# Optimization experiments

Measured on AMD Instinct MI355X. Metric: run time of the kernel, lower is better.

Reference implementation:

```python
import jax, jax.numpy as jnp
import numpy as np

N_NODES = 50000
N_EDGES = 500000
MUL0, MUL1 = 16, 8          # multiplicities of 0e and 1o irreps (in == out)
DIM = MUL0 + 3 * MUL1       # 40
N_BASIS, MID = 10, 32
WNUM = MUL0*MUL0 + MUL1*MUL0 + MUL0*MUL1 + MUL1*MUL1  # 576
INV_SQRT3 = 1.0 / np.sqrt(3.0)  # wigner-3j normalization for l=1 paths
FAN_IN = MUL0 + MUL1        # paths into each output irrep: 16 + 8 = 24
A0 = np.sqrt(1.0 / FAN_IN)  # sqrt((2*0+1)/fan_in)
A1 = np.sqrt(3.0 / FAN_IN)  # sqrt((2*1+1)/fan_in)
LN_EPS = 1e-5


def setup_inputs() -> dict:
    key = jax.random.key(0)
    ks = jax.random.split(key, 8)
    return {
        "x": jax.random.normal(ks[0], (N_NODES, DIM), jnp.float32),
        "edge_sh": jax.random.normal(ks[1], (N_EDGES, 4), jnp.float32),
        "edge_length_embedded": jax.random.uniform(ks[2], (N_EDGES, N_BASIS), jnp.float32),
        "W1": jax.random.normal(ks[3], (N_BASIS, MID), jnp.float32),
        "W2": jax.random.normal(ks[4], (MID, WNUM), jnp.float32),
        "gamma": jnp.ones((DIM,), jnp.float32),
        "beta": jnp.zeros((DIM,), jnp.float32),
        "edge_src": jax.random.randint(ks[5], (N_EDGES,), 0, N_NODES),
        "edge_dst": jax.random.randint(ks[6], (N_EDGES,), 0, N_NODES),
        "avg_num_neighbors": 10,
    }


def reference(x, edge_sh, edge_length_embedded, W1, W2, gamma, beta,
              edge_src, edge_dst, avg_num_neighbors):
    # radial MLP -> per-edge tensor-product weights (e3nn FullyConnectedNet style)
    h = jax.nn.silu(edge_length_embedded @ W1 / jnp.sqrt(jnp.float32(N_BASIS)))
    w = h @ W2 / jnp.sqrt(jnp.float32(MID))              # [E, 576]

    # gather node features onto edges and split into irrep blocks
    xg = x[edge_src]                                     # [E, 40]
    s = xg[:, :MUL0]                                     # [E, 16]  scalars 0e
    v = xg[:, MUL0:].reshape(-1, MUL1, 3)                # [E, 8, 3] vectors 1o
    sh0 = edge_sh[:, 0]                                  # [E]
    sh1 = edge_sh[:, 1:4]                                # [E, 3]

    # split per-edge weights by tensor-product path
    o0, o1, o2 = MUL0*MUL0, MUL0*MUL0 + MUL1*MUL0, MUL0*MUL0 + MUL1*MUL0 + MUL0*MUL1
    W_ss0 = w[:, :o0].reshape(-1, MUL0, MUL0)            # 0e x 0e -> 0e
    W_vv0 = w[:, o0:o1].reshape(-1, MUL1, MUL0)          # 1o x 1o -> 0e
    W_sv1 = w[:, o1:o2].reshape(-1, MUL0, MUL1)          # 0e x 1o -> 1o
    W_vs1 = w[:, o2:].reshape(-1, MUL1, MUL1)            # 1o x 0e -> 1o

    # weighted Clebsch-Gordan tensor product (per edge)
    vdot = jnp.einsum('eui,ei->eu', v, sh1) * INV_SQRT3  # CG 1x1->0
    out0 = A0 * (jnp.einsum('euk,eu->ek', W_ss0, s * sh0[:, None])
                 + jnp.einsum('euk,eu->ek', W_vv0, vdot))            # [E, 16]
    out1 = A1 * INV_SQRT3 * (
        jnp.einsum('euk,eu->ek', W_sv1, s)[:, :, None] * sh1[:, None, :]
        + jnp.einsum('euk,eui->eki', W_vs1, v) * sh0[:, None, None])  # [E, 8, 3]
    edge_values = jnp.concatenate([out0, out1.reshape(-1, 3 * MUL1)], axis=1)

    # scatter-sum into destination nodes, degree normalization, layernorm
    node = jax.ops.segment_sum(edge_values, edge_dst, num_segments=N_NODES)
    node = node / jnp.sqrt(jnp.float32(avg_num_neighbors))
    mu = node.mean(axis=-1, keepdims=True)
    var = node.var(axis=-1, keepdims=True)
    return (node - mu) * jax.lax.rsqrt(var + LN_EPS) * gamma + beta
```

## Files before the change

### kernel.cpp

```cpp
#include <hip/hip_runtime.h>
#include <hip/hip_bf16.h>

#define N_NODES 50000
#define N_EDGES 500000
#define MUL0 16
#define MUL1 8
#define DIM 40
#define N_BASIS 10
#define MID 32
#define WNUM 576
#define SCAN_BLOCKS 196
#define N_GROUPS (N_EDGES / 16)

typedef __attribute__((ext_vector_type(8))) short bf16x8_t;
typedef __attribute__((ext_vector_type(4))) float f32x4_t;

__device__ __forceinline__ float bf2f(unsigned short u) {
  return __uint_as_float(((unsigned int)u) << 16);
}
__device__ __forceinline__ unsigned short f2bf(float f) {
  unsigned int x = __float_as_uint(f);
  unsigned int r = x + 0x7fffu + ((x >> 16) & 1u);
  return (unsigned short)(r >> 16);
}
__device__ __forceinline__ bool detect_bf16(const void* gamma) {
  return ((const unsigned int*)gamma)[0] == 0x3F803F80u;
}
template <bool BF16>
__device__ __forceinline__ float ld(const void* p, size_t i) {
  if (BF16) return bf2f(((const unsigned short*)p)[i]);
  return ((const float*)p)[i];
}

#define C_INV_SQRT10 0.31622776601683794f
#define C_INV_SQRT32 0.17677669529663687f
#define C_INV_SQRT3  0.5773502691896258f
#define C_A0C        0.20412414523193154f

__device__ __forceinline__ f32x4_t mfma16x16x32(bf16x8_t a, bf16x8_t b, f32x4_t c) {
  return __builtin_amdgcn_mfma_f32_16x16x32_bf16(a, b, c, 0, 0, 0);
}


__global__ __launch_bounds__(256) void hist_kernel(
    const int* __restrict__ edge_dst, int* __restrict__ cnt) {
  int e = blockIdx.x * 256 + threadIdx.x;
  if (e < N_EDGES) atomicAdd(&cnt[edge_dst[e]], 1);
}

__global__ __launch_bounds__(256) void scanA_kernel(
    const int* __restrict__ cnt, int* __restrict__ off, int* __restrict__ btot) {
  __shared__ int s[256];
  const int tid = threadIdx.x;
  const int i = blockIdx.x * 256 + tid;
  int v = (i < N_NODES) ? cnt[i] : 0;
  s[tid] = v;
  __syncthreads();
  for (int d = 1; d < 256; d <<= 1) {
    int t = (tid >= d) ? s[tid - d] : 0;
    __syncthreads();
    s[tid] += t;
    __syncthreads();
  }
  if (i < N_NODES) off[i] = s[tid] - v;
  if (tid == 255) btot[blockIdx.x] = s[255];
}

__global__ __launch_bounds__(256) void scanB_kernel(
    const int* __restrict__ btot, int* __restrict__ bbase) {
  __shared__ int s[256];
  const int tid = threadIdx.x;
  int v = (tid < SCAN_BLOCKS) ? btot[tid] : 0;
  s[tid] = v;
  __syncthreads();
  for (int d = 1; d < 256; d <<= 1) {
    int t = (tid >= d) ? s[tid - d] : 0;
    __syncthreads();
    s[tid] += t;
    __syncthreads();
  }
  if (tid < SCAN_BLOCKS) bbase[tid] = s[tid] - v;
}

__global__ __launch_bounds__(256) void scanC_kernel(
    int* __restrict__ off, const int* __restrict__ bbase) {
  const int i = blockIdx.x * 256 + threadIdx.x;
  if (i < N_NODES) off[i] += bbase[blockIdx.x];
}

__global__ __launch_bounds__(256) void scatter_kernel(
    const int* __restrict__ edge_dst, const int* __restrict__ off,
    int* __restrict__ fill, int* __restrict__ eids) {
  int e = blockIdx.x * 256 + threadIdx.x;
  if (e >= N_EDGES) return;
  int d = edge_dst[e];
  int pos = off[d] + atomicAdd(&fill[d], 1);
  eids[pos] = e;
}


template <bool BF16>
__device__ void edge_mfma_body(
    const void* __restrict__ x,
    const void* __restrict__ edge_sh,
    const void* __restrict__ elemb,
    const void* __restrict__ W1,
    const void* __restrict__ W2,
    const int* __restrict__ edge_src,
    unsigned short* __restrict__ ev,
    short* __restrict__ w2b, float* __restrict__ w1s, float* __restrict__ stg)
{
  const int tid = threadIdx.x;

  for (int i = tid; i < 36 * 512; i += 256) {
    int m = i / WNUM;
    int col = i - m * WNUM;
    int q = m >> 3, j = m & 7;
    int t = col >> 4, n = col & 15;
    short val;
    if (BF16) val = (short)((const unsigned short*)W2)[i];
    else      val = (short)f2bf(((const float*)W2)[i]);
    w2b[t * 512 + q * 128 + n * 8 + j] = val;
  }
  for (int i = tid; i < N_BASIS * MID; i += 256) w1s[i] = ld<BF16>(W1, i);
  __syncthreads();

  const int lane = tid & 63;
  const int wid  = tid >> 6;
  const int quad = lane >> 4;
  const int l16  = lane & 15;
  float* S = stg + wid * 1504;

  for (int gi = blockIdx.x * 4 + wid; gi < N_GROUPS; gi += gridDim.x * 4) {
    const int e0 = gi * 16;

    if (lane < 16) {
      if (BF16) {
        uint2 sw = *reinterpret_cast<const uint2*>(
            (const unsigned short*)edge_sh + (size_t)(e0 + lane) * 4);
        S[0 * 16 + lane] = __uint_as_float(sw.x << 16);
        S[1 * 16 + lane] = __uint_as_float(sw.x & 0xffff0000u);
        S[2 * 16 + lane] = __uint_as_float(sw.y << 16);
        S[3 * 16 + lane] = __uint_as_float(sw.y & 0xffff0000u);
      } else {
        float4 s4 = *reinterpret_cast<const float4*>(
            (const float*)edge_sh + (size_t)(e0 + lane) * 4);
        S[0 * 16 + lane] = s4.x; S[1 * 16 + lane] = s4.y;
        S[2 * 16 + lane] = s4.z; S[3 * 16 + lane] = s4.w;
      }
    }

    {
      const int src = edge_src[e0 + l16];
      if (BF16) {
        const uint4* xr = reinterpret_cast<const uint4*>(
            (const unsigned short*)x + (size_t)src * DIM);
        uint4 c = xr[quad];
        unsigned wv[4] = {c.x, c.y, c.z, c.w};
        #pragma unroll
        for (int p = 0; p < 4; ++p) {
          int col = quad * 8 + 2 * p;
          float lo = __uint_as_float(wv[p] << 16);
          float hi = __uint_as_float(wv[p] & 0xffff0000u);
          int off0 = (col < 16) ? (64 + col * 16) : (448 + (col - 16) * 16);
          int off1 = (col + 1 < 16) ? (64 + (col + 1) * 16) : (448 + (col - 15) * 16);
          S[off0 + l16] = lo;
          S[off1 + l16] = hi;
        }
        if (lane < 16) {
          uint4 c4 = xr[4];
          unsigned wv4[4] = {c4.x, c4.y, c4.z, c4.w};
          #pragma unroll
          for (int p = 0; p < 4; ++p) {
            int col = 32 + 2 * p;
            S[448 + (col - 16) * 16 + lane] = __uint_as_float(wv4[p] << 16);
            S[448 + (col - 15) * 16 + lane] = __uint_as_float(wv4[p] & 0xffff0000u);
          }
        }
      } else {
        const float4* xr = reinterpret_cast<const float4*>(
            (const float*)x + (size_t)src * DIM);
        #pragma unroll
        for (int cc = 0; cc < 2; ++cc) {
          int c = quad + cc * 4;
          float4 t = xr[c];
          float vv[4] = {t.x, t.y, t.z, t.w};
          #pragma unroll
          for (int p = 0; p < 4; ++p) {
            int col = 4 * c + p;
            int offp = (col < 16) ? (64 + col * 16) : (448 + (col - 16) * 16);
            S[offp + l16] = vv[p];
          }
        }
        if (quad < 2) {
          int c = 8 + quad;
          float4 t = xr[c];
          float vv[4] = {t.x, t.y, t.z, t.w};
          #pragma unroll
          for (int p = 0; p < 4; ++p) {
            int col = 4 * c + p;
            S[448 + (col - 16) * 16 + l16] = vv[p];
          }
        }
      }
    }
    __builtin_amdgcn_wave_barrier();

    #pragma unroll
    for (int p = 0; p < 2; ++p) {
      int idx = lane + p * 64;
      int u = idx >> 4, e = idx & 15;
      float vdv = (S[448 + (u * 3 + 0) * 16 + e] * S[16 + e] +
                   S[448 + (u * 3 + 1) * 16 + e] * S[32 + e] +
                   S[448 + (u * 3 + 2) * 16 + e] * S[48 + e]) * C_INV_SQRT3;
      S[320 + u * 16 + e] = vdv;
    }
    __builtin_amdgcn_wave_barrier();

    bf16x8_t af;
    {
      float eb[N_BASIS];
      if (BF16) {
        const unsigned short* er = (const unsigned short*)elemb + (size_t)(e0 + l16) * N_BASIS;
        #pragma unroll
        for (int p = 0; p < 5; ++p) {
          unsigned uv = *reinterpret_cast<const unsigned*>(er + p * 2);
          eb[2 * p]     = __uint_as_float(uv << 16);
          eb[2 * p + 1] = __uint_as_float(uv & 0xffff0000u);
        }
      } else {
        const float* er = (const float*)elemb + (size_t)(e0 + l16) * N_BASIS;
        #pragma unroll
        for (int p = 0; p < 5; ++p) {
          float2 fv = *reinterpret_cast<const float2*>(er + p * 2);
          eb[2 * p] = fv.x; eb[2 * p + 1] = fv.y;
        }
      }
      #pragma unroll
      for (int j = 0; j < 8; ++j) {
        int k = quad * 8 + j;
        float p = 0.f;
        #pragma unroll
        for (int b = 0; b < N_BASIS; ++b) p += eb[b] * w1s[b * MID + k];
        float z = p * C_INV_SQRT10;
        float hh = z / (1.f + __expf(-z)) * C_INV_SQRT32;
        af[j] = (short)f2bf(hh);
      }
    }

    f32x4_t s0 = *reinterpret_cast<const f32x4_t*>(&S[quad * 4]);

    f32x4_t out0 = {0.f, 0.f, 0.f, 0.f};
    f32x4_t tsv  = {0.f, 0.f, 0.f, 0.f};
    f32x4_t tv0  = {0.f, 0.f, 0.f, 0.f};
    f32x4_t tv1  = {0.f, 0.f, 0.f, 0.f};
    f32x4_t tv2  = {0.f, 0.f, 0.f, 0.f};
    const f32x4_t zero = {0.f, 0.f, 0.f, 0.f};
    const int usel = (l16 >> 3);

    #pragma unroll
    for (int t = 0; t < 16; ++t) {
      bf16x8_t bf = *reinterpret_cast<const bf16x8_t*>(&w2b[t * 512 + lane * 8]);
      f32x4_t D = mfma16x16x32(af, bf, zero);
      f32x4_t sv = *reinterpret_cast<const f32x4_t*>(&S[64 + t * 16 + quad * 4]);
      out0 += D * (sv * s0);
    }
    #pragma unroll
    for (int t = 0; t < 8; ++t) {
      bf16x8_t bf = *reinterpret_cast<const bf16x8_t*>(&w2b[(16 + t) * 512 + lane * 8]);
      f32x4_t D = mfma16x16x32(af, bf, zero);
      f32x4_t vdv = *reinterpret_cast<const f32x4_t*>(&S[320 + t * 16 + quad * 4]);
      out0 += D * vdv;
    }
    #pragma unroll
    for (int t = 0; t < 8; ++t) {
      bf16x8_t bf = *reinterpret_cast<const bf16x8_t*>(&w2b[(24 + t) * 512 + lane * 8]);
      f32x4_t D = mfma16x16x32(af, bf, zero);
      int u = 2 * t + usel;
      f32x4_t sv = *reinterpret_cast<const f32x4_t*>(&S[64 + u * 16 + quad * 4]);
      tsv += D * sv;
    }
    #pragma unroll
    for (int t = 0; t < 4; ++t) {
      bf16x8_t bf = *reinterpret_cast<const bf16x8_t*>(&w2b[(32 + t) * 512 + lane * 8]);
      f32x4_t D = mfma16x16x32(af, bf, zero);
      int u = 2 * t + usel;
      f32x4_t v0 = *reinterpret_cast<const f32x4_t*>(&S[448 + (u * 3 + 0) * 16 + quad * 4]);
      f32x4_t v1 = *reinterpret_cast<const f32x4_t*>(&S[448 + (u * 3 + 1) * 16 + quad * 4]);
      f32x4_t v2 = *reinterpret_cast<const f32x4_t*>(&S[448 + (u * 3 + 2) * 16 + quad * 4]);
      tv0 += D * v0; tv1 += D * v1; tv2 += D * v2;
    }

    #pragma unroll
    for (int r = 0; r < 4; ++r) {
      tsv[r] += __shfl_xor(tsv[r], 8, 64);
      tv0[r] += __shfl_xor(tv0[r], 8, 64);
      tv1[r] += __shfl_xor(tv1[r], 8, 64);
      tv2[r] += __shfl_xor(tv2[r], 8, 64);
    }

    #pragma unroll
    for (int r = 0; r < 4; ++r)
      S[832 + (quad * 4 + r) * 42 + l16] = C_A0C * out0[r];
    if (l16 < 8) {
      f32x4_t h1x = *reinterpret_cast<const f32x4_t*>(&S[16 + quad * 4]);
      f32x4_t h1y = *reinterpret_cast<const f32x4_t*>(&S[32 + quad * 4]);
      f32x4_t h1z = *reinterpret_cast<const f32x4_t*>(&S[48 + quad * 4]);
      #pragma unroll
      for (int r = 0; r < 4; ++r) {
        int rowb = 832 + (quad * 4 + r) * 42 + 16 + 3 * l16;
        S[rowb + 0] = C_A0C * (tsv[r] * h1x[r] + tv0[r] * s0[r]);
        S[rowb + 1] = C_A0C * (tsv[r] * h1y[r] + tv1[r] * s0[r]);
        S[rowb + 2] = C_A0C * (tsv[r] * h1z[r] + tv2[r] * s0[r]);
      }
    }
    __builtin_amdgcn_wave_barrier();

    unsigned* evout = reinterpret_cast<unsigned*>(ev + (size_t)e0 * DIM);
    #pragma unroll
    for (int sI = 0; sI < 5; ++sI) {
      int vidx = 2 * (lane + 64 * sI);
      int edge = vidx / 40, col = vidx - edge * 40;
      float2 pr = *reinterpret_cast<const float2*>(&S[832 + edge * 42 + col]);
      evout[lane + 64 * sI] = (unsigned)f2bf(pr.x) | ((unsigned)f2bf(pr.y) << 16);
    }
  }
}

__global__ __launch_bounds__(256, 2) void edge_mfma_kernel(
    const void* __restrict__ x,
    const void* __restrict__ edge_sh,
    const void* __restrict__ elemb,
    const void* __restrict__ W1,
    const void* __restrict__ W2,
    const void* __restrict__ gamma,
    const int* __restrict__ edge_src,
    unsigned short* __restrict__ ev)
{
  __shared__ __align__(16) short w2b[36 * 512];
  __shared__ __align__(16) float w1s[N_BASIS * MID];
  __shared__ __align__(16) float stg[4 * 1504];

  if (detect_bf16(gamma))
    edge_mfma_body<true >(x, edge_sh, elemb, W1, W2, edge_src, ev, w2b, w1s, stg);
  else
    edge_mfma_body<false>(x, edge_sh, elemb, W1, W2, edge_src, ev, w2b, w1s, stg);
}


template <bool BF16>
__device__ __forceinline__ void node_body(
    const unsigned short* __restrict__ ev,
    const int* __restrict__ eids,
    const int* __restrict__ cnt,
    const int* __restrict__ off,
    const void* __restrict__ gamma,
    const void* __restrict__ beta,
    const int* __restrict__ avg,
    void* __restrict__ out, int n)
{
  const int c = cnt[n];
  const int o = off[n];
  float s[DIM];
  #pragma unroll
  for (int d = 0; d < DIM; ++d) s[d] = 0.f;

  for (int j = 0; j < c; ++j) {
    int e = eids[o + j];
    const uint4* p = reinterpret_cast<const uint4*>(ev + (size_t)e * DIM);
    #pragma unroll
    for (int q = 0; q < 5; ++q) {
      uint4 t = p[q];
      unsigned int wl[4] = {t.x, t.y, t.z, t.w};
      #pragma unroll
      for (int r = 0; r < 4; ++r) {
        s[q * 8 + 2 * r]     += __uint_as_float(wl[r] << 16);
        s[q * 8 + 2 * r + 1] += __uint_as_float(wl[r] & 0xffff0000u);
      }
    }
  }

  const float inv = rsqrtf((float)avg[0]);
  float mean = 0.f;
  #pragma unroll
  for (int d = 0; d < DIM; ++d) { s[d] *= inv; mean += s[d]; }
  mean *= (1.f / DIM);
  float var = 0.f;
  #pragma unroll
  for (int d = 0; d < DIM; ++d) { float dd = s[d] - mean; var += dd * dd; }
  var *= (1.f / DIM);
  const float r = rsqrtf(var + 1e-5f);

  if (BF16) {
    #pragma unroll
    for (int d = 0; d < DIM; ++d) {
      float y = (s[d] - mean) * r * ld<true>(gamma, d) + ld<true>(beta, d);
      ((unsigned short*)out)[(size_t)n * DIM + d] = f2bf(y);
    }
  } else {
    float4* op = reinterpret_cast<float4*>((float*)out + (size_t)n * DIM);
    #pragma unroll
    for (int q = 0; q < 10; ++q) {
      float4 t;
      t.x = (s[q*4+0] - mean) * r * ld<false>(gamma, q*4+0) + ld<false>(beta, q*4+0);
      t.y = (s[q*4+1] - mean) * r * ld<false>(gamma, q*4+1) + ld<false>(beta, q*4+1);
      t.z = (s[q*4+2] - mean) * r * ld<false>(gamma, q*4+2) + ld<false>(beta, q*4+2);
      t.w = (s[q*4+3] - mean) * r * ld<false>(gamma, q*4+3) + ld<false>(beta, q*4+3);
      op[q] = t;
    }
  }
}

__global__ __launch_bounds__(256) void node_kernel(
    const unsigned short* __restrict__ ev,
    const int* __restrict__ eids,
    const int* __restrict__ cnt,
    const int* __restrict__ off,
    const void* __restrict__ gamma,
    const void* __restrict__ beta,
    const int* __restrict__ avg,
    void* __restrict__ out)
{
  const int n = blockIdx.x * blockDim.x + threadIdx.x;
  if (n >= N_NODES) return;
  if (detect_bf16(gamma)) node_body<true >(ev, eids, cnt, off, gamma, beta, avg, out, n);
  else                    node_body<false>(ev, eids, cnt, off, gamma, beta, avg, out, n);
}

extern "C" void kernel_launch(void* const* d_in, const int* in_sizes, int n_in,
                              void* d_out, int out_size, void* d_ws, size_t ws_size,
                              hipStream_t stream) {
  const void* x       = d_in[0];
  const void* edge_sh = d_in[1];
  const void* elemb   = d_in[2];
  const void* W1      = d_in[3];
  const void* W2      = d_in[4];
  const void* gamma   = d_in[5];
  const void* beta    = d_in[6];
  const int* edge_src = (const int*)d_in[7];
  const int* edge_dst = (const int*)d_in[8];
  const int* avg      = (const int*)d_in[9];

  char* wsb = (char*)d_ws;
  unsigned short* ev = (unsigned short*)(wsb);
  int* eids  = (int*)(wsb + 40000000);
  int* cnt   = (int*)(wsb + 42000000);
  int* off   = (int*)(wsb + 42200000);
  int* fill  = (int*)(wsb + 42400000);
  int* btot  = (int*)(wsb + 42600000);
  int* bbase = (int*)(wsb + 42600800);

  hipMemsetAsync(cnt, 0, 600000, stream);

  const int EB = (N_EDGES + 255) / 256;
  hist_kernel   <<<EB, 256, 0, stream>>>(edge_dst, cnt);
  scanA_kernel  <<<SCAN_BLOCKS, 256, 0, stream>>>(cnt, off, btot);
  scanB_kernel  <<<1, 256, 0, stream>>>(btot, bbase);
  scanC_kernel  <<<SCAN_BLOCKS, 256, 0, stream>>>(off, bbase);
  scatter_kernel<<<EB, 256, 0, stream>>>(edge_dst, off, fill, eids);

  edge_mfma_kernel<<<512, 256, 0, stream>>>(x, edge_sh, elemb, W1, W2, gamma,
                                            edge_src, ev);

  node_kernel<<<SCAN_BLOCKS, 256, 0, stream>>>(ev, eids, cnt, off,
                                               gamma, beta, avg, d_out);
}
```

Measured before the change: 239.1 us.

## Write edge values in destination-sorted order so node reduction reads contiguously

The position kernel now records each edge's slot in the CSR order rather than an edge-id list. The edge kernel scatters its bf16 output rows straight to those slots, so the node kernel reads each node's edges as one contiguous block without the eids indirection. The LDS staging buffer is shrunk by reusing the front of the per-wave area, which allows occupancy 3 and a 768-block grid. The cost is scattered 16-byte writes from the edge kernel in place of coalesced stores, plus extra wave barriers to guard the reused LDS.

```diff
diff --git a/kernel.cpp b/kernel.cpp
--- a/kernel.cpp
+++ b/kernel.cpp
@@ -88,14 +88,13 @@
   if (i < N_NODES) off[i] += bbase[blockIdx.x];
 }
 
-__global__ __launch_bounds__(256) void scatter_kernel(
+__global__ __launch_bounds__(256) void pos_kernel(
     const int* __restrict__ edge_dst, const int* __restrict__ off,
-    int* __restrict__ fill, int* __restrict__ eids) {
+    int* __restrict__ fill, int* __restrict__ epos) {
   int e = blockIdx.x * 256 + threadIdx.x;
   if (e >= N_EDGES) return;
   int d = edge_dst[e];
-  int pos = off[d] + atomicAdd(&fill[d], 1);
-  eids[pos] = e;
+  epos[e] = off[d] + atomicAdd(&fill[d], 1);
 }
 
 
@@ -107,6 +106,7 @@
     const void* __restrict__ W1,
     const void* __restrict__ W2,
     const int* __restrict__ edge_src,
+    const int* __restrict__ epos,
     unsigned short* __restrict__ ev,
     short* __restrict__ w2b, float* __restrict__ w1s, float* __restrict__ stg)
 {
@@ -129,10 +129,14 @@
   const int wid  = tid >> 6;
   const int quad = lane >> 4;
   const int l16  = lane & 15;
-  float* S = stg + wid * 1504;
+  float* S = stg + wid * 832;
 
   for (int gi = blockIdx.x * 4 + wid; gi < N_GROUPS; gi += gridDim.x * 4) {
     const int e0 = gi * 16;
+    __builtin_amdgcn_wave_barrier();
+
+    const int posA = epos[e0 + (lane >> 2)];
+    const int posB = (lane < 16) ? epos[e0 + lane] : 0;
 
     if (lane < 16) {
       if (BF16) {
@@ -298,17 +302,18 @@
       tv1[r] += __shfl_xor(tv1[r], 8, 64);
       tv2[r] += __shfl_xor(tv2[r], 8, 64);
     }
+    __builtin_amdgcn_wave_barrier();
 
     #pragma unroll
     for (int r = 0; r < 4; ++r)
-      S[832 + (quad * 4 + r) * 42 + l16] = C_A0C * out0[r];
+      S[64 + (quad * 4 + r) * 42 + l16] = C_A0C * out0[r];
     if (l16 < 8) {
       f32x4_t h1x = *reinterpret_cast<const f32x4_t*>(&S[16 + quad * 4]);
       f32x4_t h1y = *reinterpret_cast<const f32x4_t*>(&S[32 + quad * 4]);
       f32x4_t h1z = *reinterpret_cast<const f32x4_t*>(&S[48 + quad * 4]);
       #pragma unroll
       for (int r = 0; r < 4; ++r) {
-        int rowb = 832 + (quad * 4 + r) * 42 + 16 + 3 * l16;
+        int rowb = 64 + (quad * 4 + r) * 42 + 16 + 3 * l16;
         S[rowb + 0] = C_A0C * (tsv[r] * h1x[r] + tv0[r] * s0[r]);
         S[rowb + 1] = C_A0C * (tsv[r] * h1y[r] + tv1[r] * s0[r]);
         S[rowb + 2] = C_A0C * (tsv[r] * h1z[r] + tv2[r] * s0[r]);
@@ -316,18 +321,29 @@
     }
     __builtin_amdgcn_wave_barrier();
 
-    unsigned* evout = reinterpret_cast<unsigned*>(ev + (size_t)e0 * DIM);
-    #pragma unroll
-    for (int sI = 0; sI < 5; ++sI) {
-      int vidx = 2 * (lane + 64 * sI);
-      int edge = vidx / 40, col = vidx - edge * 40;
-      float2 pr = *reinterpret_cast<const float2*>(&S[832 + edge * 42 + col]);
-      evout[lane + 64 * sI] = (unsigned)f2bf(pr.x) | ((unsigned)f2bf(pr.y) << 16);
-    }
-  }
-}
-
-__global__ __launch_bounds__(256, 2) void edge_mfma_kernel(
+    {
+      const int edge = lane >> 2, chunk = lane & 3;
+      const float* rp = &S[64 + edge * 42 + chunk * 8];
+      unsigned p0 = (unsigned)f2bf(rp[0]) | ((unsigned)f2bf(rp[1]) << 16);
+      unsigned p1 = (unsigned)f2bf(rp[2]) | ((unsigned)f2bf(rp[3]) << 16);
+      unsigned p2 = (unsigned)f2bf(rp[4]) | ((unsigned)f2bf(rp[5]) << 16);
+      unsigned p3 = (unsigned)f2bf(rp[6]) | ((unsigned)f2bf(rp[7]) << 16);
+      uint4 t; t.x = p0; t.y = p1; t.z = p2; t.w = p3;
+      *reinterpret_cast<uint4*>(ev + (size_t)posA * DIM + chunk * 8) = t;
+      if (lane < 16) {
+        const float* rq = &S[64 + lane * 42 + 32];
+        unsigned q0 = (unsigned)f2bf(rq[0]) | ((unsigned)f2bf(rq[1]) << 16);
+        unsigned q1 = (unsigned)f2bf(rq[2]) | ((unsigned)f2bf(rq[3]) << 16);
+        unsigned q2 = (unsigned)f2bf(rq[4]) | ((unsigned)f2bf(rq[5]) << 16);
+        unsigned q3 = (unsigned)f2bf(rq[6]) | ((unsigned)f2bf(rq[7]) << 16);
+        uint4 t2; t2.x = q0; t2.y = q1; t2.z = q2; t2.w = q3;
+        *reinterpret_cast<uint4*>(ev + (size_t)posB * DIM + 32) = t2;
+      }
+    }
+  }
+}
+
+__global__ __launch_bounds__(256, 3) void edge_mfma_kernel(
     const void* __restrict__ x,
     const void* __restrict__ edge_sh,
     const void* __restrict__ elemb,
@@ -335,23 +351,23 @@
     const void* __restrict__ W2,
     const void* __restrict__ gamma,
     const int* __restrict__ edge_src,
+    const int* __restrict__ epos,
     unsigned short* __restrict__ ev)
 {
   __shared__ __align__(16) short w2b[36 * 512];
   __shared__ __align__(16) float w1s[N_BASIS * MID];
-  __shared__ __align__(16) float stg[4 * 1504];
+  __shared__ __align__(16) float stg[4 * 832];
 
   if (detect_bf16(gamma))
-    edge_mfma_body<true >(x, edge_sh, elemb, W1, W2, edge_src, ev, w2b, w1s, stg);
+    edge_mfma_body<true >(x, edge_sh, elemb, W1, W2, edge_src, epos, ev, w2b, w1s, stg);
   else
-    edge_mfma_body<false>(x, edge_sh, elemb, W1, W2, edge_src, ev, w2b, w1s, stg);
+    edge_mfma_body<false>(x, edge_sh, elemb, W1, W2, edge_src, epos, ev, w2b, w1s, stg);
 }
 
 
 template <bool BF16>
 __device__ __forceinline__ void node_body(
     const unsigned short* __restrict__ ev,
-    const int* __restrict__ eids,
     const int* __restrict__ cnt,
     const int* __restrict__ off,
     const void* __restrict__ gamma,
@@ -365,12 +381,11 @@
   #pragma unroll
   for (int d = 0; d < DIM; ++d) s[d] = 0.f;
 
+  const uint4* p = reinterpret_cast<const uint4*>(ev + (size_t)o * DIM);
   for (int j = 0; j < c; ++j) {
-    int e = eids[o + j];
-    const uint4* p = reinterpret_cast<const uint4*>(ev + (size_t)e * DIM);
     #pragma unroll
     for (int q = 0; q < 5; ++q) {
-      uint4 t = p[q];
+      uint4 t = p[j * 5 + q];
       unsigned int wl[4] = {t.x, t.y, t.z, t.w};
       #pragma unroll
       for (int r = 0; r < 4; ++r) {
@@ -413,7 +428,6 @@
 
 __global__ __launch_bounds__(256) void node_kernel(
     const unsigned short* __restrict__ ev,
-    const int* __restrict__ eids,
     const int* __restrict__ cnt,
     const int* __restrict__ off,
     const void* __restrict__ gamma,
@@ -423,8 +437,8 @@
 {
   const int n = blockIdx.x * blockDim.x + threadIdx.x;
   if (n >= N_NODES) return;
-  if (detect_bf16(gamma)) node_body<true >(ev, eids, cnt, off, gamma, beta, avg, out, n);
-  else                    node_body<false>(ev, eids, cnt, off, gamma, beta, avg, out, n);
+  if (detect_bf16(gamma)) node_body<true >(ev, cnt, off, gamma, beta, avg, out, n);
+  else                    node_body<false>(ev, cnt, off, gamma, beta, avg, out, n);
 }
 
 extern "C" void kernel_launch(void* const* d_in, const int* in_sizes, int n_in,
@@ -443,25 +457,25 @@
 
   char* wsb = (char*)d_ws;
   unsigned short* ev = (unsigned short*)(wsb);
-  int* eids  = (int*)(wsb + 40000000);
+  int* epos  = (int*)(wsb + 40000000);
   int* cnt   = (int*)(wsb + 42000000);
-  int* off   = (int*)(wsb + 42200000);
-  int* fill  = (int*)(wsb + 42400000);
+  int* fill  = (int*)(wsb + 42200000);
+  int* off   = (int*)(wsb + 42400000);
   int* btot  = (int*)(wsb + 42600000);
   int* bbase = (int*)(wsb + 42600800);
 
-  hipMemsetAsync(cnt, 0, 600000, stream);
+  hipMemsetAsync(cnt, 0, 400000, stream);
 
   const int EB = (N_EDGES + 255) / 256;
-  hist_kernel   <<<EB, 256, 0, stream>>>(edge_dst, cnt);
-  scanA_kernel  <<<SCAN_BLOCKS, 256, 0, stream>>>(cnt, off, btot);
-  scanB_kernel  <<<1, 256, 0, stream>>>(btot, bbase);
-  scanC_kernel  <<<SCAN_BLOCKS, 256, 0, stream>>>(off, bbase);
-  scatter_kernel<<<EB, 256, 0, stream>>>(edge_dst, off, fill, eids);
-
-  edge_mfma_kernel<<<512, 256, 0, stream>>>(x, edge_sh, elemb, W1, W2, gamma,
-                                            edge_src, ev);
-
-  node_kernel<<<SCAN_BLOCKS, 256, 0, stream>>>(ev, eids, cnt, off,
+  hist_kernel <<<EB, 256, 0, stream>>>(edge_dst, cnt);
+  scanA_kernel<<<SCAN_BLOCKS, 256, 0, stream>>>(cnt, off, btot);
+  scanB_kernel<<<1, 256, 0, stream>>>(btot, bbase);
+  scanC_kernel<<<SCAN_BLOCKS, 256, 0, stream>>>(off, bbase);
+  pos_kernel  <<<EB, 256, 0, stream>>>(edge_dst, off, fill, epos);
+
+  edge_mfma_kernel<<<768, 256, 0, stream>>>(x, edge_sh, elemb, W1, W2, gamma,
+                                            edge_src, epos, ev);
+
+  node_kernel<<<SCAN_BLOCKS, 256, 0, stream>>>(ev, cnt, off,
                                                gamma, beta, avg, d_out);
 }
```

New measurement: 241.8 us. About the same (+1.1%).
